# Kernel tuning notes

Hardware: AMD Instinct MI355X
Metric: run time of the kernel (lower is better)

The kernel has to match this reference:

```python
import jax, jax.numpy as jnp
import numpy as np
import random

EPS = 1e-16  # matches EKM eps default
B, M, N, R = 8, 8192, 512, 256


def setup_inputs() -> dict:
    key = jax.random.key(0)
    kx, = jax.random.split(key, 1)
    x = jax.random.normal(kx, (B, M, N), dtype=jnp.float32)
    # EKM init: random.seed(42); inds = random.sample(range(M), R)
    random.seed(42)
    inds = jnp.asarray(random.sample(range(M), R), dtype=jnp.int32)
    # EKMInit overrides ekm.alpha with nn.Parameter(torch.tensor([0.1]))
    alpha = jnp.asarray([0.1], dtype=jnp.float32)
    return {"x": x, "alpha": alpha, "inds": inds}


def _memberships(x, v, alpha):
    x2 = jnp.sum(x * x, axis=2, keepdims=True)           # (B, M, 1)
    xv = jnp.einsum('bmn,bnr->bmr', x, v)                # (B, M, R)
    v2 = jnp.sum(v * v, axis=1, keepdims=True)           # (B, 1, R)
    d = jax.nn.relu(x2 - 2.0 * xv + v2)
    return jax.nn.softmax(-d / alpha, axis=2)            # (B, M, R)


def reference(x, alpha, inds):
    # init: v0 = t(x[:, inds, :]) -> (B, N, R); u0 = memberships(x, v0)
    v0 = jnp.swapaxes(x[:, inds, :], 1, 2)               # (B, N, R)
    # solver step (num_iters=1): u_new = memberships(x, v0) (== u0),
    # v_new = centers(x, u_new)
    u = _memberships(x, v0, alpha)                       # (B, M, R)
    u_n = (u + EPS) / (jnp.sum(u, axis=1, keepdims=True) + EPS)
    v = jnp.einsum('bmn,bmr->bnr', x, u_n)               # (B, N, R)
    return (u, v)
```

## Files before the change

kernel.cpp:

```cpp
#include <hip/hip_runtime.h>
#include <math.h>

#define B 8
#define M 8192
#define N 512
#define R 256
#define EPSF 1e-16f

typedef __attribute__((ext_vector_type(8))) short short8;
typedef __attribute__((ext_vector_type(16))) float f32x16;

__device__ __forceinline__ unsigned short bf16_rtn(float f) {
    unsigned int u = __float_as_uint(f);
    u += 0x7FFFu + ((u >> 16) & 1u);
    return (unsigned short)(u >> 16);
}

__device__ __forceinline__ void gll16(const unsigned short* g, unsigned short* l) {
    __builtin_amdgcn_global_load_lds(
        (const __attribute__((address_space(1))) unsigned int*)g,
        (__attribute__((address_space(3))) unsigned int*)l, 16, 0, 0);
}

__global__ __launch_bounds__(256) void ekm_kc(
    const float* __restrict__ x, const int* __restrict__ inds,
    unsigned short* __restrict__ c_hi, unsigned short* __restrict__ c_lo,
    float* __restrict__ v2g)
{
    const int t = threadIdx.x, b = blockIdx.y;
    const int r = blockIdx.x * 16 + (t >> 4);
    const int seg = (t & 15) * 32;
    const float* src = x + ((size_t)b * M + inds[r]) * N + seg;
    unsigned short* hd = c_hi + ((size_t)b * R + r) * 512 + seg;
    unsigned short* ld = c_lo + ((size_t)b * R + r) * 512 + seg;
    float vp = 0.f;
#pragma unroll
    for (int c = 0; c < 4; ++c) {
        float4 f0 = *(const float4*)(src + c * 8);
        float4 f1 = *(const float4*)(src + c * 8 + 4);
        float av[8] = {f0.x, f0.y, f0.z, f0.w, f1.x, f1.y, f1.z, f1.w};
        unsigned ph[4], pl[4];
#pragma unroll
        for (int j = 0; j < 4; ++j) {
            vp += av[2*j] * av[2*j] + av[2*j+1] * av[2*j+1];
            unsigned short h0 = bf16_rtn(av[2*j]), h1 = bf16_rtn(av[2*j+1]);
            float r0 = av[2*j]   - __uint_as_float((unsigned)h0 << 16);
            float r1 = av[2*j+1] - __uint_as_float((unsigned)h1 << 16);
            ph[j] = (unsigned)h0 | ((unsigned)h1 << 16);
            pl[j] = (unsigned)bf16_rtn(r0) | ((unsigned)bf16_rtn(r1) << 16);
        }
        *(uint4*)(hd + c * 8) = make_uint4(ph[0], ph[1], ph[2], ph[3]);
        *(uint4*)(ld + c * 8) = make_uint4(pl[0], pl[1], pl[2], pl[3]);
    }
    vp += __shfl_xor(vp, 1); vp += __shfl_xor(vp, 2);
    vp += __shfl_xor(vp, 4); vp += __shfl_xor(vp, 8);
    if ((t & 15) == 0) v2g[b * R + r] = vp;
}

__global__ __launch_bounds__(256, 3) void ekm_k1(
    const float* __restrict__ x, const float* __restrict__ alpha_p,
    const unsigned short* __restrict__ c_hi, const unsigned short* __restrict__ c_lo,
    const float* __restrict__ v2g, float* __restrict__ u_out,
    unsigned short* __restrict__ uT, unsigned short* __restrict__ xT,
    float* __restrict__ colsum)
{
    __shared__ unsigned short Ah[64 * 40], Al[64 * 40];
    __shared__ unsigned short Bh[256 * 32], Bl[256 * 32];
    __shared__ float x2s[64];
    __shared__ float redm[4][64], reds[4][64];

    const int t = threadIdx.x;
    const int b = blockIdx.y;
    const int m0 = blockIdx.x * 64;
    const int w = t >> 6, l = t & 63, col = l & 31, h5 = l >> 5;
    const int arow = t >> 2, kch = t & 3;
    const int cswz = (t & 3) ^ ((t >> 3) & 3);
    const int pswz = (col >> 1) & 3;

    const float* ax = x + ((size_t)b * M + m0 + arow) * N + kch * 8;
    const unsigned short* bhs = c_hi + ((size_t)b * R + (t >> 2)) * 512 + cswz * 8;
    const unsigned short* bls = c_lo + ((size_t)b * R + (t >> 2)) * 512 + cswz * 8;

    f32x16 acc[2][2];
    acc[0][0] = (f32x16)0.f; acc[0][1] = (f32x16)0.f;
    acc[1][0] = (f32x16)0.f; acc[1][1] = (f32x16)0.f;

    float x2p = 0.f;
    float4 a0 = *(const float4*)(ax);
    float4 a1 = *(const float4*)(ax + 4);

    for (int k0 = 0; k0 < N; k0 += 32) {
        x2p += a0.x*a0.x + a0.y*a0.y + a0.z*a0.z + a0.w*a0.w
             + a1.x*a1.x + a1.y*a1.y + a1.z*a1.z + a1.w*a1.w;
        float av[8] = {a0.x, a0.y, a0.z, a0.w, a1.x, a1.y, a1.z, a1.w};
        unsigned ph[4], pl[4];
#pragma unroll
        for (int j = 0; j < 4; ++j) {
            unsigned short h0 = bf16_rtn(av[2*j]), h1 = bf16_rtn(av[2*j+1]);
            float r0 = av[2*j]   - __uint_as_float((unsigned)h0 << 16);
            float r1 = av[2*j+1] - __uint_as_float((unsigned)h1 << 16);
            ph[j] = (unsigned)h0 | ((unsigned)h1 << 16);
            pl[j] = (unsigned)bf16_rtn(r0) | ((unsigned)bf16_rtn(r1) << 16);
        }
        __syncthreads();
#pragma unroll
        for (int i = 0; i < 4; ++i) {
            gll16(bhs + k0 + i * (64 * 512), Bh + i * 2048 + t * 8);
            gll16(bls + k0 + i * (64 * 512), Bl + i * 2048 + t * 8);
        }
        *(uint4*)&Ah[arow * 40 + kch * 8] = make_uint4(ph[0], ph[1], ph[2], ph[3]);
        *(uint4*)&Al[arow * 40 + kch * 8] = make_uint4(pl[0], pl[1], pl[2], pl[3]);
        __syncthreads();

        if (k0 + 32 < N) {
            a0 = *(const float4*)(ax + k0 + 32);
            a1 = *(const float4*)(ax + k0 + 36);
        }

        {
            int kk = t >> 3, ms = (t & 7) * 8;
            unsigned q0 = (unsigned)Ah[(ms+0)*40+kk] | ((unsigned)Ah[(ms+1)*40+kk] << 16);
            unsigned q1 = (unsigned)Ah[(ms+2)*40+kk] | ((unsigned)Ah[(ms+3)*40+kk] << 16);
            unsigned q2 = (unsigned)Ah[(ms+4)*40+kk] | ((unsigned)Ah[(ms+5)*40+kk] << 16);
            unsigned q3 = (unsigned)Ah[(ms+6)*40+kk] | ((unsigned)Ah[(ms+7)*40+kk] << 16);
            *(uint4*)(xT + ((size_t)b * N + k0 + kk) * M + m0 + ms) = make_uint4(q0, q1, q2, q3);
        }

#pragma unroll
        for (int half = 0; half < 2; ++half) {
            const int pc = (half * 2 + h5) ^ pswz;
            short8 ah[2], al2[2], bh[2], bl2[2];
#pragma unroll
            for (int tm = 0; tm < 2; ++tm) {
                ah[tm]  = *(const short8*)&Ah[(tm*32 + col) * 40 + half*16 + h5*8];
                al2[tm] = *(const short8*)&Al[(tm*32 + col) * 40 + half*16 + h5*8];
            }
#pragma unroll
            for (int tr = 0; tr < 2; ++tr) {
                bh[tr]  = *(const short8*)&Bh[(w*64 + tr*32 + col) * 32 + pc*8];
                bl2[tr] = *(const short8*)&Bl[(w*64 + tr*32 + col) * 32 + pc*8];
            }
#pragma unroll
            for (int tm = 0; tm < 2; ++tm)
#pragma unroll
            for (int tr = 0; tr < 2; ++tr) {
                acc[tm][tr] = __builtin_amdgcn_mfma_f32_32x32x16_bf16(ah[tm],  bh[tr],  acc[tm][tr], 0, 0, 0);
                acc[tm][tr] = __builtin_amdgcn_mfma_f32_32x32x16_bf16(ah[tm],  bl2[tr], acc[tm][tr], 0, 0, 0);
                acc[tm][tr] = __builtin_amdgcn_mfma_f32_32x32x16_bf16(al2[tm], bh[tr],  acc[tm][tr], 0, 0, 0);
            }
        }
    }

    x2p += __shfl_xor(x2p, 1);
    x2p += __shfl_xor(x2p, 2);
    if (kch == 0) x2s[arow] = x2p;
    __syncthreads();

    const float ia = 1.4426950408889634f / alpha_p[0];
    float v2c[2];
#pragma unroll
    for (int tr = 0; tr < 2; ++tr)
        v2c[tr] = v2g[b * R + w * 64 + tr * 32 + col];

#pragma unroll
    for (int tm = 0; tm < 2; ++tm)
#pragma unroll
    for (int reg = 0; reg < 16; ++reg) {
        int rowl = (reg & 3) + 8 * (reg >> 2) + 4 * h5;
        float x2v = x2s[tm * 32 + rowl];
        float mn;
#pragma unroll
        for (int tr = 0; tr < 2; ++tr) {
            float d = x2v - 2.f * acc[tm][tr][reg] + v2c[tr];
            d = fmaxf(d, 0.f);
            acc[tm][tr][reg] = d;
            mn = (tr == 0) ? d : fminf(mn, d);
        }
        mn = fminf(mn, __shfl_xor(mn, 1));
        mn = fminf(mn, __shfl_xor(mn, 2));
        mn = fminf(mn, __shfl_xor(mn, 4));
        mn = fminf(mn, __shfl_xor(mn, 8));
        mn = fminf(mn, __shfl_xor(mn, 16));
        if (col == 0) redm[w][tm * 32 + rowl] = mn;
    }
    __syncthreads();

#pragma unroll
    for (int tm = 0; tm < 2; ++tm)
#pragma unroll
    for (int reg = 0; reg < 16; ++reg) {
        int m = tm * 32 + (reg & 3) + 8 * (reg >> 2) + 4 * h5;
        float mn = fminf(fminf(redm[0][m], redm[1][m]), fminf(redm[2][m], redm[3][m]));
        float s = 0.f;
#pragma unroll
        for (int tr = 0; tr < 2; ++tr) {
            float e = exp2f((mn - acc[tm][tr][reg]) * ia);
            acc[tm][tr][reg] = e;
            s += e;
        }
        s += __shfl_xor(s, 1); s += __shfl_xor(s, 2); s += __shfl_xor(s, 4);
        s += __shfl_xor(s, 8); s += __shfl_xor(s, 16);
        if (col == 0) reds[w][m] = s;
    }
    __syncthreads();

    float* ub = u_out + ((size_t)b * M + m0) * R + w * 64;
    float cs[2] = {0.f, 0.f};
#pragma unroll
    for (int tm = 0; tm < 2; ++tm)
#pragma unroll
    for (int reg = 0; reg < 16; ++reg) {
        int rowl = (reg & 3) + 8 * (reg >> 2) + 4 * h5;
        int m = tm * 32 + rowl;
        float inv = 1.f / (reds[0][m] + reds[1][m] + reds[2][m] + reds[3][m]);
#pragma unroll
        for (int tr = 0; tr < 2; ++tr) {
            float uu = acc[tm][tr][reg] * inv;
            acc[tm][tr][reg] = uu;
            ub[(size_t)m * R + tr * 32 + col] = uu;
            cs[tr] += uu;
        }
    }
    unsigned short* uTb = uT + ((size_t)b * R + w * 64) * M + m0;
#pragma unroll
    for (int tm = 0; tm < 2; ++tm)
#pragma unroll
    for (int tr = 0; tr < 2; ++tr)
#pragma unroll
    for (int rq = 0; rq < 4; ++rq) {
        uint2 p;
        p.x = (unsigned)bf16_rtn(acc[tm][tr][rq*4+0]) | ((unsigned)bf16_rtn(acc[tm][tr][rq*4+1]) << 16);
        p.y = (unsigned)bf16_rtn(acc[tm][tr][rq*4+2]) | ((unsigned)bf16_rtn(acc[tm][tr][rq*4+3]) << 16);
        *(uint2*)(uTb + (size_t)(tr*32 + col) * M + tm*32 + 8*rq + 4*h5) = p;
    }
    cs[0] += __shfl_xor(cs[0], 32);
    cs[1] += __shfl_xor(cs[1], 32);
    if (h5 == 0) {
        atomicAdd(&colsum[b * R + w * 64 + col], cs[0]);
        atomicAdd(&colsum[b * R + w * 64 + 32 + col], cs[1]);
    }
}

__global__ __launch_bounds__(256, 2) void ekm_k2(
    const unsigned short* __restrict__ xT, const unsigned short* __restrict__ uT,
    float* __restrict__ part)
{
    __shared__ unsigned short XA[128 * 32], UB[128 * 32];
    const int t = threadIdx.x;
    const int nt = blockIdx.x >> 1, rt = blockIdx.x & 1;
    const int slab = blockIdx.y, b = blockIdx.z;
    const int n0 = nt * 128, r0 = rt * 128;
    const int w = t >> 6, l = t & 63, col = l & 31, h5 = l >> 5;
    const int wn = w >> 1, wr = w & 1;
    const int cswz = (t & 3) ^ ((t >> 3) & 3);
    const int pswz = (col >> 1) & 3;

    const unsigned short* xs = xT + ((size_t)b * N + n0 + (t >> 2)) * M + slab * 1024 + cswz * 8;
    const unsigned short* us = uT + ((size_t)b * R + r0 + (t >> 2)) * M + slab * 1024 + cswz * 8;

    f32x16 acc[2][2];
    acc[0][0] = (f32x16)0.f; acc[0][1] = (f32x16)0.f;
    acc[1][0] = (f32x16)0.f; acc[1][1] = (f32x16)0.f;

    for (int k0 = 0; k0 < 1024; k0 += 32) {
        __syncthreads();
#pragma unroll
        for (int i = 0; i < 2; ++i) {
            gll16(xs + k0 + (size_t)i * 64 * M, XA + i * 2048 + t * 8);
            gll16(us + k0 + (size_t)i * 64 * M, UB + i * 2048 + t * 8);
        }
        __syncthreads();
#pragma unroll
        for (int half = 0; half < 2; ++half) {
            const int pc = (half * 2 + h5) ^ pswz;
            short8 af[2], bf2[2];
#pragma unroll
            for (int tm = 0; tm < 2; ++tm)
                af[tm] = *(const short8*)&XA[(wn*64 + tm*32 + col) * 32 + pc*8];
#pragma unroll
            for (int tr = 0; tr < 2; ++tr)
                bf2[tr] = *(const short8*)&UB[(wr*64 + tr*32 + col) * 32 + pc*8];
#pragma unroll
            for (int tm = 0; tm < 2; ++tm)
#pragma unroll
            for (int tr = 0; tr < 2; ++tr)
                acc[tm][tr] = __builtin_amdgcn_mfma_f32_32x32x16_bf16(af[tm], bf2[tr], acc[tm][tr], 0, 0, 0);
        }
    }

    float* pb = part + (size_t)slab * ((size_t)B * N * R) + (size_t)b * N * R;
#pragma unroll
    for (int tm = 0; tm < 2; ++tm)
#pragma unroll
    for (int reg = 0; reg < 16; ++reg) {
        int n = n0 + wn*64 + tm*32 + (reg & 3) + 8*(reg >> 2) + 4*h5;
#pragma unroll
        for (int tr = 0; tr < 2; ++tr)
            pb[(size_t)n * R + r0 + wr*64 + tr*32 + col] = acc[tm][tr][reg];
    }
}

__global__ __launch_bounds__(256) void ekm_red(
    const float* __restrict__ part, const float* __restrict__ colsum,
    float* __restrict__ v_out)
{
    size_t o = ((size_t)blockIdx.x * 256 + threadIdx.x) * 4;
    float sx = 0.f, sy = 0.f, sz = 0.f, sw = 0.f;
#pragma unroll
    for (int sl = 0; sl < 8; ++sl) {
        float4 p = *(const float4*)(part + (size_t)sl * B * N * R + o);
        sx += p.x; sy += p.y; sz += p.z; sw += p.w;
    }
    int b = (int)(o >> 17);
    int r = (int)(o & (R - 1));
    float4 cs = *(const float4*)(colsum + b * R + r);
    float4 vo;
    vo.x = sx / (cs.x + EPSF);
    vo.y = sy / (cs.y + EPSF);
    vo.z = sz / (cs.z + EPSF);
    vo.w = sw / (cs.w + EPSF);
    *(float4*)(v_out + o) = vo;
}

extern "C" void kernel_launch(void* const* d_in, const int* in_sizes, int n_in,
                              void* d_out, int out_size, void* d_ws, size_t ws_size,
                              hipStream_t stream) {
    const float* x     = (const float*)d_in[0];
    const float* alpha = (const float*)d_in[1];
    const int*   inds  = (const int*)d_in[2];

    float* u_out = (float*)d_out;
    float* v_out = u_out + (size_t)B * M * R;

    char* ws = (char*)d_ws;
    const size_t CH = (size_t)B * R * 512 * 2;
    unsigned short* c_hi   = (unsigned short*)ws;
    unsigned short* c_lo   = (unsigned short*)(ws + CH);
    float*          v2g    = (float*)(ws + 2 * CH);
    float*          colsum = (float*)(ws + 2 * CH + (size_t)B * R * 4);
    char* p = ws + 2 * CH + 2 * (size_t)B * R * 4;
    unsigned short* xT = (unsigned short*)p;          p += (size_t)B * N * M * 2;
    unsigned short* uT = (unsigned short*)p;          p += (size_t)B * R * M * 2;
    float*          part = (float*)p;

    hipMemsetAsync(colsum, 0, (size_t)B * R * sizeof(float), stream);

    ekm_kc<<<dim3(16, B), 256, 0, stream>>>(x, inds, c_hi, c_lo, v2g);
    ekm_k1<<<dim3(M / 64, B), 256, 0, stream>>>(x, alpha, c_hi, c_lo, v2g,
                                                u_out, uT, xT, colsum);
    ekm_k2<<<dim3(8, 8, B), 256, 0, stream>>>(xT, uT, part);
    ekm_red<<<(B * N * R / 4) / 256, 256, 0, stream>>>(part, colsum, v_out);
}
```

Measured before the change: 349.2 us.

## Double-buffer LDS tiles and software-pipeline global loads in both GEMM kernels

After: 348.2 us. About the same (-0.3%).

```diff
diff --git a/kernel.cpp b/kernel.cpp
--- a/kernel.cpp
+++ b/kernel.cpp
@@ -57,17 +57,15 @@
     if ((t & 15) == 0) v2g[b * R + r] = vp;
 }
 
-__global__ __launch_bounds__(256, 3) void ekm_k1(
+__global__ __launch_bounds__(256, 2) void ekm_k1(
     const float* __restrict__ x, const float* __restrict__ alpha_p,
     const unsigned short* __restrict__ c_hi, const unsigned short* __restrict__ c_lo,
     const float* __restrict__ v2g, float* __restrict__ u_out,
     unsigned short* __restrict__ uT, unsigned short* __restrict__ xT,
     float* __restrict__ colsum)
 {
-    __shared__ unsigned short Ah[64 * 40], Al[64 * 40];
-    __shared__ unsigned short Bh[256 * 32], Bl[256 * 32];
-    __shared__ float x2s[64];
-    __shared__ float redm[4][64], reds[4][64];
+    __shared__ unsigned short Bh[2][8192], Bl[2][8192];
+    __shared__ unsigned short Ah[2][2048], Al[2][2048];
 
     const int t = threadIdx.x;
     const int b = blockIdx.y;
@@ -76,6 +74,7 @@
     const int arow = t >> 2, kch = t & 3;
     const int cswz = (t & 3) ^ ((t >> 3) & 3);
     const int pswz = (col >> 1) & 3;
+    const int aws = arow * 32 + (kch ^ ((arow >> 1) & 3)) * 8;
 
     const float* ax = x + ((size_t)b * M + m0 + arow) * N + kch * 8;
     const unsigned short* bhs = c_hi + ((size_t)b * R + (t >> 2)) * 512 + cswz * 8;
@@ -86,70 +85,112 @@
     acc[1][0] = (f32x16)0.f; acc[1][1] = (f32x16)0.f;
 
     float x2p = 0.f;
-    float4 a0 = *(const float4*)(ax);
-    float4 a1 = *(const float4*)(ax + 4);
-
-    for (int k0 = 0; k0 < N; k0 += 32) {
-        x2p += a0.x*a0.x + a0.y*a0.y + a0.z*a0.z + a0.w*a0.w
-             + a1.x*a1.x + a1.y*a1.y + a1.z*a1.z + a1.w*a1.w;
+    unsigned ph[4], pl[4];
+    float4 a0, a1;
+
+    auto convert = [&](void) {
         float av[8] = {a0.x, a0.y, a0.z, a0.w, a1.x, a1.y, a1.z, a1.w};
-        unsigned ph[4], pl[4];
 #pragma unroll
         for (int j = 0; j < 4; ++j) {
+            x2p += av[2*j] * av[2*j] + av[2*j+1] * av[2*j+1];
             unsigned short h0 = bf16_rtn(av[2*j]), h1 = bf16_rtn(av[2*j+1]);
             float r0 = av[2*j]   - __uint_as_float((unsigned)h0 << 16);
             float r1 = av[2*j+1] - __uint_as_float((unsigned)h1 << 16);
             ph[j] = (unsigned)h0 | ((unsigned)h1 << 16);
             pl[j] = (unsigned)bf16_rtn(r0) | ((unsigned)bf16_rtn(r1) << 16);
         }
-        __syncthreads();
-#pragma unroll
-        for (int i = 0; i < 4; ++i) {
-            gll16(bhs + k0 + i * (64 * 512), Bh + i * 2048 + t * 8);
-            gll16(bls + k0 + i * (64 * 512), Bl + i * 2048 + t * 8);
-        }
-        *(uint4*)&Ah[arow * 40 + kch * 8] = make_uint4(ph[0], ph[1], ph[2], ph[3]);
-        *(uint4*)&Al[arow * 40 + kch * 8] = make_uint4(pl[0], pl[1], pl[2], pl[3]);
-        __syncthreads();
-
-        if (k0 + 32 < N) {
-            a0 = *(const float4*)(ax + k0 + 32);
-            a1 = *(const float4*)(ax + k0 + 36);
-        }
-
-        {
-            int kk = t >> 3, ms = (t & 7) * 8;
-            unsigned q0 = (unsigned)Ah[(ms+0)*40+kk] | ((unsigned)Ah[(ms+1)*40+kk] << 16);
-            unsigned q1 = (unsigned)Ah[(ms+2)*40+kk] | ((unsigned)Ah[(ms+3)*40+kk] << 16);
-            unsigned q2 = (unsigned)Ah[(ms+4)*40+kk] | ((unsigned)Ah[(ms+5)*40+kk] << 16);
-            unsigned q3 = (unsigned)Ah[(ms+6)*40+kk] | ((unsigned)Ah[(ms+7)*40+kk] << 16);
-            *(uint4*)(xT + ((size_t)b * N + k0 + kk) * M + m0 + ms) = make_uint4(q0, q1, q2, q3);
-        }
-
+    };
+
+    auto mfma_tile = [&](int c) {
 #pragma unroll
         for (int half = 0; half < 2; ++half) {
             const int pc = (half * 2 + h5) ^ pswz;
-            short8 ah[2], al2[2], bh[2], bl2[2];
+            short8 ahf[2], alf[2], bhf[2], blf[2];
 #pragma unroll
             for (int tm = 0; tm < 2; ++tm) {
-                ah[tm]  = *(const short8*)&Ah[(tm*32 + col) * 40 + half*16 + h5*8];
-                al2[tm] = *(const short8*)&Al[(tm*32 + col) * 40 + half*16 + h5*8];
+                ahf[tm] = *(const short8*)&Ah[c][(tm*32 + col) * 32 + pc * 8];
+                alf[tm] = *(const short8*)&Al[c][(tm*32 + col) * 32 + pc * 8];
             }
 #pragma unroll
             for (int tr = 0; tr < 2; ++tr) {
-                bh[tr]  = *(const short8*)&Bh[(w*64 + tr*32 + col) * 32 + pc*8];
-                bl2[tr] = *(const short8*)&Bl[(w*64 + tr*32 + col) * 32 + pc*8];
+                bhf[tr] = *(const short8*)&Bh[c][(w*64 + tr*32 + col) * 32 + pc * 8];
+                blf[tr] = *(const short8*)&Bl[c][(w*64 + tr*32 + col) * 32 + pc * 8];
             }
 #pragma unroll
             for (int tm = 0; tm < 2; ++tm)
 #pragma unroll
             for (int tr = 0; tr < 2; ++tr) {
-                acc[tm][tr] = __builtin_amdgcn_mfma_f32_32x32x16_bf16(ah[tm],  bh[tr],  acc[tm][tr], 0, 0, 0);
-                acc[tm][tr] = __builtin_amdgcn_mfma_f32_32x32x16_bf16(ah[tm],  bl2[tr], acc[tm][tr], 0, 0, 0);
-                acc[tm][tr] = __builtin_amdgcn_mfma_f32_32x32x16_bf16(al2[tm], bh[tr],  acc[tm][tr], 0, 0, 0);
+                acc[tm][tr] = __builtin_amdgcn_mfma_f32_32x32x16_bf16(ahf[tm], bhf[tr], acc[tm][tr], 0, 0, 0);
+                acc[tm][tr] = __builtin_amdgcn_mfma_f32_32x32x16_bf16(ahf[tm], blf[tr], acc[tm][tr], 0, 0, 0);
+                acc[tm][tr] = __builtin_amdgcn_mfma_f32_32x32x16_bf16(alf[tm], bhf[tr], acc[tm][tr], 0, 0, 0);
             }
         }
-    }
+    };
+
+    auto xt_store = [&](int c, int tt) {
+        int kk = t >> 3, ms = (t & 7) * 8;
+        unsigned short vv[8];
+#pragma unroll
+        for (int i = 0; i < 8; ++i) {
+            int row = ms + i;
+            vv[i] = Ah[c][row * 32 + (((kk >> 3) ^ ((row >> 1) & 3)) << 3) + (kk & 7)];
+        }
+        *(uint4*)(xT + ((size_t)b * N + tt * 32 + kk) * M + m0 + ms) =
+            make_uint4((unsigned)vv[0] | ((unsigned)vv[1] << 16),
+                       (unsigned)vv[2] | ((unsigned)vv[3] << 16),
+                       (unsigned)vv[4] | ((unsigned)vv[5] << 16),
+                       (unsigned)vv[6] | ((unsigned)vv[7] << 16));
+    };
+
+    a0 = *(const float4*)(ax);
+    a1 = *(const float4*)(ax + 4);
+    convert();
+#pragma unroll
+    for (int i = 0; i < 4; ++i) {
+        gll16(bhs + i * (64 * 512), &Bh[0][i * 2048 + t * 8]);
+        gll16(bls + i * (64 * 512), &Bl[0][i * 2048 + t * 8]);
+    }
+    __builtin_amdgcn_sched_barrier(0);
+    *(uint4*)&Ah[0][aws] = make_uint4(ph[0], ph[1], ph[2], ph[3]);
+    *(uint4*)&Al[0][aws] = make_uint4(pl[0], pl[1], pl[2], pl[3]);
+    a0 = *(const float4*)(ax + 32);
+    a1 = *(const float4*)(ax + 36);
+    asm volatile("s_waitcnt vmcnt(2) lgkmcnt(0)" ::: "memory");
+    __builtin_amdgcn_s_barrier();
+    __builtin_amdgcn_sched_barrier(0);
+
+    auto body = [&](int tt, int c, int nb) {
+        convert();
+#pragma unroll
+        for (int i = 0; i < 4; ++i) {
+            gll16(bhs + (tt + 1) * 32 + i * (64 * 512), &Bh[nb][i * 2048 + t * 8]);
+            gll16(bls + (tt + 1) * 32 + i * (64 * 512), &Bl[nb][i * 2048 + t * 8]);
+        }
+        __builtin_amdgcn_sched_barrier(0);
+        *(uint4*)&Ah[nb][aws] = make_uint4(ph[0], ph[1], ph[2], ph[3]);
+        *(uint4*)&Al[nb][aws] = make_uint4(pl[0], pl[1], pl[2], pl[3]);
+        const int pf = (tt + 2 < 16 ? tt + 2 : 15) * 32;
+        a0 = *(const float4*)(ax + pf);
+        a1 = *(const float4*)(ax + pf + 4);
+        xt_store(c, tt);
+        mfma_tile(c);
+        asm volatile("s_waitcnt vmcnt(3) lgkmcnt(0)" ::: "memory");
+        __builtin_amdgcn_s_barrier();
+        __builtin_amdgcn_sched_barrier(0);
+    };
+
+#pragma unroll 1
+    for (int tp = 0; tp < 7; ++tp) {
+        body(2 * tp, 0, 1);
+        body(2 * tp + 1, 1, 0);
+    }
+    body(14, 0, 1);
+    mfma_tile(1);
+    xt_store(1, 15);
+
+    float* x2s = (float*)&Al[0][0];
+    float (*redm)[64] = (float (*)[64])&Bh[0][0];
+    float (*reds)[64] = (float (*)[64])&Bh[0][2048];
 
     x2p += __shfl_xor(x2p, 1);
     x2p += __shfl_xor(x2p, 2);
@@ -245,48 +286,72 @@
     const unsigned short* __restrict__ xT, const unsigned short* __restrict__ uT,
     float* __restrict__ part)
 {
-    __shared__ unsigned short XA[128 * 32], UB[128 * 32];
+    __shared__ unsigned short XA[2][8192], UB[2][8192];
     const int t = threadIdx.x;
     const int nt = blockIdx.x >> 1, rt = blockIdx.x & 1;
     const int slab = blockIdx.y, b = blockIdx.z;
     const int n0 = nt * 128, r0 = rt * 128;
     const int w = t >> 6, l = t & 63, col = l & 31, h5 = l >> 5;
     const int wn = w >> 1, wr = w & 1;
-    const int cswz = (t & 3) ^ ((t >> 3) & 3);
-    const int pswz = (col >> 1) & 3;
-
-    const unsigned short* xs = xT + ((size_t)b * N + n0 + (t >> 2)) * M + slab * 1024 + cswz * 8;
-    const unsigned short* us = uT + ((size_t)b * R + r0 + (t >> 2)) * M + slab * 1024 + cswz * 8;
+    const int srow = t >> 3;
+    const int chunk = (t & 7) ^ (srow & 7);
+    const int rx = col & 7;
+
+    const unsigned short* xs = xT + ((size_t)b * N + n0 + srow) * M + (size_t)slab * 1024 + chunk * 8;
+    const unsigned short* us = uT + ((size_t)b * R + r0 + srow) * M + (size_t)slab * 1024 + chunk * 8;
 
     f32x16 acc[2][2];
     acc[0][0] = (f32x16)0.f; acc[0][1] = (f32x16)0.f;
     acc[1][0] = (f32x16)0.f; acc[1][1] = (f32x16)0.f;
 
-    for (int k0 = 0; k0 < 1024; k0 += 32) {
-        __syncthreads();
-#pragma unroll
-        for (int i = 0; i < 2; ++i) {
-            gll16(xs + k0 + (size_t)i * 64 * M, XA + i * 2048 + t * 8);
-            gll16(us + k0 + (size_t)i * 64 * M, UB + i * 2048 + t * 8);
-        }
-        __syncthreads();
-#pragma unroll
-        for (int half = 0; half < 2; ++half) {
-            const int pc = (half * 2 + h5) ^ pswz;
+#pragma unroll
+    for (int i = 0; i < 4; ++i) {
+        gll16(xs + (size_t)i * 32 * M, &XA[0][i * 2048 + t * 8]);
+        gll16(us + (size_t)i * 32 * M, &UB[0][i * 2048 + t * 8]);
+    }
+    asm volatile("s_waitcnt vmcnt(0)" ::: "memory");
+    __builtin_amdgcn_s_barrier();
+    __builtin_amdgcn_sched_barrier(0);
+
+    auto body = [&](int tt, int c, int nb, bool stage) {
+        if (stage) {
+#pragma unroll
+            for (int i = 0; i < 4; ++i) {
+                gll16(xs + (tt + 1) * 64 + (size_t)i * 32 * M, &XA[nb][i * 2048 + t * 8]);
+                gll16(us + (tt + 1) * 64 + (size_t)i * 32 * M, &UB[nb][i * 2048 + t * 8]);
+            }
+            __builtin_amdgcn_sched_barrier(0);
+        }
+#pragma unroll
+        for (int kk = 0; kk < 4; ++kk) {
+            const int pc = (kk * 2 + h5) ^ rx;
             short8 af[2], bf2[2];
 #pragma unroll
             for (int tm = 0; tm < 2; ++tm)
-                af[tm] = *(const short8*)&XA[(wn*64 + tm*32 + col) * 32 + pc*8];
+                af[tm] = *(const short8*)&XA[c][(wn*64 + tm*32 + col) * 64 + pc * 8];
 #pragma unroll
             for (int tr = 0; tr < 2; ++tr)
-                bf2[tr] = *(const short8*)&UB[(wr*64 + tr*32 + col) * 32 + pc*8];
+                bf2[tr] = *(const short8*)&UB[c][(wr*64 + tr*32 + col) * 64 + pc * 8];
 #pragma unroll
             for (int tm = 0; tm < 2; ++tm)
 #pragma unroll
             for (int tr = 0; tr < 2; ++tr)
                 acc[tm][tr] = __builtin_amdgcn_mfma_f32_32x32x16_bf16(af[tm], bf2[tr], acc[tm][tr], 0, 0, 0);
         }
-    }
+        if (stage) {
+            asm volatile("s_waitcnt vmcnt(0)" ::: "memory");
+            __builtin_amdgcn_s_barrier();
+            __builtin_amdgcn_sched_barrier(0);
+        }
+    };
+
+#pragma unroll 1
+    for (int tp = 0; tp < 7; ++tp) {
+        body(2 * tp, 0, 1, true);
+        body(2 * tp + 1, 1, 0, true);
+    }
+    body(14, 0, 1, true);
+    body(15, 1, 0, false);
 
     float* pb = part + (size_t)slab * ((size_t)B * N * R) + (size_t)b * N * R;
 #pragma unroll
```
